# Performance work log

Measured on AMD Instinct MI355X. Metric: run time of the kernel, lower is better.

Reference implementation:

```python
import jax, jax.numpy as jnp
import numpy as np

N_NODES = 50000
N_EDGES = 800000
D = 128
L = 3


def setup_inputs() -> dict:
    key = jax.random.key(0)
    ks = jax.random.split(key, 16)
    x = jax.random.normal(ks[0], (N_NODES, D), dtype=jnp.float32)
    edge_index = jax.random.randint(ks[1], (2, N_EDGES), 0, N_NODES, dtype=jnp.int32)
    # ensure every node has at least one incoming edge (degree > 0)
    edge_index = edge_index.at[1, :N_NODES].set(jnp.arange(N_NODES, dtype=jnp.int32))
    edge_attr = jax.random.normal(ks[2], (N_EDGES, 1), dtype=jnp.float32)
    s = 1.0 / np.sqrt(D)
    lin_w = jax.random.normal(ks[3], (L, 1, D), dtype=jnp.float32)          # edge_dim=1 -> D
    lin_b = jax.random.normal(ks[4], (L, D), dtype=jnp.float32) * s
    eps = jnp.zeros((L,), dtype=jnp.float32)                                 # initial_eps = 0, trainable
    w1 = jax.random.normal(ks[5], (L, D, D), dtype=jnp.float32) * s
    b1 = jax.random.normal(ks[6], (L, D), dtype=jnp.float32) * s
    w2 = jax.random.normal(ks[7], (L, D, D), dtype=jnp.float32) * s
    b2 = jax.random.normal(ks[8], (L, D), dtype=jnp.float32) * s
    d_cat = D + L * D
    final_w = jax.random.normal(ks[9], (d_cat, D), dtype=jnp.float32) / np.sqrt(d_cat)
    final_b = jax.random.normal(ks[10], (D,), dtype=jnp.float32) * s
    return {"x": x, "edge_index": edge_index, "edge_attr": edge_attr,
            "lin_w": lin_w, "lin_b": lin_b, "eps": eps,
            "w1": w1, "b1": b1, "w2": w2, "b2": b2,
            "final_w": final_w, "final_b": final_b}


def reference(x, edge_index, edge_attr, lin_w, lin_b, eps, w1, b1, w2, b2, final_w, final_b):
    src, tgt = edge_index[0], edge_index[1]
    n = x.shape[0]
    # degree of target nodes (float), shape [N, 1]
    deg = jax.ops.segment_sum(jnp.ones(src.shape[0], x.dtype), tgt, num_segments=n)[:, None]
    xs = [x]
    h = x
    for l in range(L):
        e = edge_attr @ lin_w[l] + lin_b[l]                  # [E, D] edge-feature projection
        msg = jax.nn.relu(h[src] + e)                        # gather + fuse + relu
        agg = jax.ops.segment_sum(msg, tgt, num_segments=n)  # scatter-add
        out = agg / deg + (1.0 + eps[l]) * h                 # degree-normalize + eps-residual
        h = jax.nn.relu(out @ w1[l] + b1[l]) @ w2[l] + b2[l] # 2-layer MLP (no BN, no dropout)
        xs.append(h)
    cat = jnp.concatenate(xs, axis=-1)                       # [N, D + L*D]
    return cat @ final_w + final_b
```

## Files before the change

### kernel.cpp

```cpp
#include <hip/hip_runtime.h>

#define NN 50000
#define NE 800000
#define DIM 128
#define NLAYERS 3

typedef __attribute__((ext_vector_type(8))) short bf16x8;
typedef __attribute__((ext_vector_type(4))) float f32x4;

__device__ __forceinline__ unsigned short f2bf_hi(float f) {
    unsigned int u = __float_as_uint(f);
    u += 0x7FFF + ((u >> 16) & 1);
    return (unsigned short)(u >> 16);
}
__device__ __forceinline__ float bf2f(unsigned short u) {
    return __uint_as_float(((unsigned int)u) << 16);
}

__global__ __launch_bounds__(256) void rank_kernel(const int* __restrict__ tgt,
                                                   int* __restrict__ counts,
                                                   int* __restrict__ rank, int E) {
    int base = (blockIdx.x * 256 + threadIdx.x) * 4;
    if (base >= E) return;
    int4 t = *(const int4*)(tgt + base);
    int4 r;
    r.x = atomicAdd(&counts[t.x], 1);
    r.y = atomicAdd(&counts[t.y], 1);
    r.z = atomicAdd(&counts[t.z], 1);
    r.w = atomicAdd(&counts[t.w], 1);
    *(int4*)(rank + base) = r;
}

__global__ __launch_bounds__(256) void scan_partial_kernel(const int* __restrict__ counts,
                                                           int* __restrict__ psum, int n) {
    __shared__ int ws[4];
    int b = blockIdx.x, t = threadIdx.x;
    int idx = b * 1024 + t * 4;
    int v = 0;
    if (idx < n) {
        int4 c = *(const int4*)(counts + idx);
        v = c.x + c.y + c.z + c.w;
    }
#pragma unroll
    for (int o = 32; o > 0; o >>= 1) v += __shfl_xor(v, o);
    int lane = t & 63, wid = t >> 6;
    if (lane == 0) ws[wid] = v;
    __syncthreads();
    if (t == 0) psum[b] = ws[0] + ws[1] + ws[2] + ws[3];
}

__global__ __launch_bounds__(64) void scan_small_kernel(const int* __restrict__ psum,
                                                        int* __restrict__ pbase,
                                                        int* __restrict__ offsets,
                                                        int nb, int n) {
    int lane = threadIdx.x;
    int v = (lane < nb) ? psum[lane] : 0;
    int incl = v;
#pragma unroll
    for (int o = 1; o < 64; o <<= 1) {
        int t = __shfl_up(incl, o);
        if (lane >= o) incl += t;
    }
    if (lane < nb) pbase[lane] = incl - v;
    if (lane == 63) offsets[n] = incl;
}

__global__ __launch_bounds__(256) void scan_apply_kernel(const int* __restrict__ counts,
                                                         const int* __restrict__ pbase,
                                                         int* __restrict__ offsets, int n) {
    __shared__ int ws[4];
    int b = blockIdx.x, t = threadIdx.x;
    int lane = t & 63, wid = t >> 6;
    int idx = b * 1024 + t * 4;
    int4 c = make_int4(0, 0, 0, 0);
    if (idx < n) c = *(const int4*)(counts + idx);
    int tsum = c.x + c.y + c.z + c.w;
    int incl = tsum;
#pragma unroll
    for (int o = 1; o < 64; o <<= 1) {
        int tt = __shfl_up(incl, o);
        if (lane >= o) incl += tt;
    }
    if (lane == 63) ws[wid] = incl;
    __syncthreads();
    int wbase = pbase[b];
    for (int w = 0; w < wid; w++) wbase += ws[w];
    if (idx < n) {
        int e0 = wbase + incl - tsum;
        int4 o;
        o.x = e0;
        o.y = e0 + c.x;
        o.z = o.y + c.y;
        o.w = o.z + c.z;
        *(int4*)(offsets + idx) = o;
    }
}

__global__ __launch_bounds__(256) void scatter2_kernel(
    const int* __restrict__ src, const int* __restrict__ tgt,
    const float* __restrict__ ea, const int* __restrict__ rank,
    const int* __restrict__ offsets, int2* __restrict__ sedge, int E) {
    int base = (blockIdx.x * 256 + threadIdx.x) * 4;
    if (base >= E) return;
    int4 s = *(const int4*)(src + base);
    int4 t = *(const int4*)(tgt + base);
    int4 r = *(const int4*)(rank + base);
    float4 a = *(const float4*)(ea + base);
    sedge[offsets[t.x] + r.x] = make_int2(s.x << 8, __float_as_int(a.x));
    sedge[offsets[t.y] + r.y] = make_int2(s.y << 8, __float_as_int(a.y));
    sedge[offsets[t.z] + r.z] = make_int2(s.z << 8, __float_as_int(a.z));
    sedge[offsets[t.w] + r.w] = make_int2(s.w << 8, __float_as_int(a.w));
}

__global__ __launch_bounds__(256) void xcvt_kernel(const float* __restrict__ x,
                                                   unsigned short* __restrict__ xb, int n) {
    int i = (blockIdx.x * 256 + threadIdx.x) * 4;
    if (i >= n) return;
    float4 v = *(const float4*)(x + i);
    ushort4 o;
    o.x = f2bf_hi(v.x); o.y = f2bf_hi(v.y);
    o.z = f2bf_hi(v.z); o.w = f2bf_hi(v.w);
    *(ushort4*)(xb + i) = o;
}

__global__ __launch_bounds__(256, 8) void agg_kernel(
    const unsigned short* __restrict__ hprev, const int* __restrict__ offs,
    const int2* __restrict__ sedge,
    const float* __restrict__ lw, const float* __restrict__ lb,
    const float* __restrict__ epsp, int layer,
    unsigned short* __restrict__ aggh, unsigned short* __restrict__ aggl, int N) {
    int g = threadIdx.x >> 4;
    int r = threadIdx.x & 15;
    int node = blockIdx.x * 16 + g;
    if (node >= N) return;
    int d0 = r * 8;
    float lwv[8], lbv[8];
    *(float4*)&lwv[0] = *(const float4*)(lw + d0);
    *(float4*)&lwv[4] = *(const float4*)(lw + d0 + 4);
    *(float4*)&lbv[0] = *(const float4*)(lb + d0);
    *(float4*)&lbv[4] = *(const float4*)(lb + d0 + 4);
    const char* hb = (const char*)hprev + r * 16;

    int s0 = offs[node], s1 = offs[node + 1];
    int sm = s1 - 1;
    int cnt = s1 - s0;
    float a[8];
#pragma unroll
    for (int c = 0; c < 8; c++) a[c] = 0.f;

    int2 e0 = sedge[s0];
    int2 e1 = sedge[min(s0 + 1, sm)];
    int2 e2 = sedge[min(s0 + 2, sm)];
    int2 e3 = sedge[min(s0 + 3, sm)];
    uint4 h0 = *(const uint4*)(hb + (unsigned)e0.x);
    uint4 h1 = *(const uint4*)(hb + (unsigned)e1.x);
    uint4 h2 = *(const uint4*)(hb + (unsigned)e2.x);

    for (int it = s0; it < s1; ++it) {
        uint4 h3 = *(const uint4*)(hb + (unsigned)e3.x);
        int2 e4 = sedge[min(it + 4, sm)];
        float wgt = __int_as_float(e0.y);
        unsigned uu[4] = {h0.x, h0.y, h0.z, h0.w};
#pragma unroll
        for (int c = 0; c < 4; c++) {
            float f0 = __uint_as_float(uu[c] << 16);
            float f1 = __uint_as_float(uu[c] & 0xffff0000u);
            a[2 * c]     += fmaxf(f0 + fmaf(wgt, lwv[2 * c], lbv[2 * c]), 0.f);
            a[2 * c + 1] += fmaxf(f1 + fmaf(wgt, lwv[2 * c + 1], lbv[2 * c + 1]), 0.f);
        }
        e0 = e1; e1 = e2; e2 = e3; e3 = e4;
        h0 = h1; h1 = h2; h2 = h3;
    }

    float inv = 1.f / (float)cnt;
    float ge = 1.f + epsp[layer];
    uint4 hs = *(const uint4*)(hb + ((unsigned)node << 8));
    unsigned su[4] = {hs.x, hs.y, hs.z, hs.w};
    unsigned short hh[8], hl[8];
#pragma unroll
    for (int c = 0; c < 4; c++) {
        float f0 = __uint_as_float(su[c] << 16);
        float f1 = __uint_as_float(su[c] & 0xffff0000u);
        float v0 = a[2 * c] * inv + ge * f0;
        float v1 = a[2 * c + 1] * inv + ge * f1;
        unsigned short h0v = f2bf_hi(v0), h1v = f2bf_hi(v1);
        hh[2 * c] = h0v; hh[2 * c + 1] = h1v;
        hl[2 * c] = f2bf_hi(v0 - bf2f(h0v));
        hl[2 * c + 1] = f2bf_hi(v1 - bf2f(h1v));
    }
    unsigned short* ph = aggh + (size_t)node * DIM + d0;
    unsigned short* pl = aggl + (size_t)node * DIM + d0;
    *(ushort4*)ph       = *(const ushort4*)&hh[0];
    *(ushort4*)(ph + 4) = *(const ushort4*)&hh[4];
    *(ushort4*)pl       = *(const ushort4*)&hl[0];
    *(ushort4*)(pl + 4) = *(const ushort4*)&hl[4];
}

__device__ __forceinline__ int packidx(int k, int c) {
    return (((k >> 5) << 3) + (c >> 4)) * 512 + (((k >> 3) & 3) << 7) + ((c & 15) << 3) + (k & 7);
}

__global__ __launch_bounds__(256) void wprep_kernel(
    const float* __restrict__ w1, const float* __restrict__ w2, const float* __restrict__ fw,
    unsigned short* __restrict__ w1t_h, unsigned short* __restrict__ w1t_l,
    unsigned short* __restrict__ w2t_h, unsigned short* __restrict__ w2t_l,
    unsigned short* __restrict__ fwt_h, unsigned short* __restrict__ fwt_l) {
    int gid = blockIdx.x * 256 + threadIdx.x;
    float v; int oidx;
    unsigned short *oh, *ol;
    if (gid < 49152) {
        int l = gid >> 14, rem = gid & 16383, k = rem >> 7, c = rem & 127;
        v = w1[gid]; oidx = l * 16384 + packidx(k, c); oh = w1t_h; ol = w1t_l;
    } else if (gid < 98304) {
        int g = gid - 49152;
        int l = g >> 14, rem = g & 16383, k = rem >> 7, c = rem & 127;
        v = w2[g]; oidx = l * 16384 + packidx(k, c); oh = w2t_h; ol = w2t_l;
    } else if (gid < 163840) {
        int g = gid - 98304;
        int k = g >> 7, c = g & 127;
        v = fw[g]; oidx = packidx(k, c); oh = fwt_h; ol = fwt_l;
    } else return;
    unsigned short h = f2bf_hi(v);
    float lo = v - bf2f(h);
    oh[oidx] = h;
    ol[oidx] = f2bf_hi(lo);
}

#define HSTR 136

__global__ __launch_bounds__(256, 4) void mlp_fused(
    const unsigned short* __restrict__ ah_g, const unsigned short* __restrict__ al_g,
    const unsigned short* __restrict__ w1h, const unsigned short* __restrict__ w1l,
    const float* __restrict__ b1,
    const unsigned short* __restrict__ w2h, const unsigned short* __restrict__ w2l,
    const float* __restrict__ b2,
    unsigned short* __restrict__ out, int N) {
    __shared__ unsigned short s_hh[64 * HSTR], s_hl[64 * HSTR];
    int tid = threadIdx.x;
    int lane = tid & 63, w = tid >> 6;
    int q = lane >> 4, lr = lane & 15;
    int wr = w >> 1, wc = w & 1;
    int n0 = blockIdx.x * 64;
    int nb0 = n0 + wc * 32 + lr;

    f32x4 acc[4][2];
#pragma unroll
    for (int i = 0; i < 4; i++)
#pragma unroll
        for (int j = 0; j < 2; j++) acc[i][j] = (f32x4)(0.f);

#pragma unroll
    for (int k0 = 0; k0 < 128; k0 += 32) {
        bf16x8 Bh[2], Bl[2];
#pragma unroll
        for (int j = 0; j < 2; j++) {
            size_t ro = (size_t)min(nb0 + j * 16, N - 1) * DIM + k0 + q * 8;
            Bh[j] = *(const bf16x8*)(ah_g + ro);
            Bl[j] = *(const bf16x8*)(al_g + ro);
        }
#pragma unroll
        for (int i = 0; i < 4; i++) {
            size_t co = ((size_t)((k0 >> 5) * 8 + wr * 4 + i) << 9) + lane * 8;
            bf16x8 Ah = *(const bf16x8*)(w1h + co);
            bf16x8 Al = *(const bf16x8*)(w1l + co);
#pragma unroll
            for (int j = 0; j < 2; j++) {
                acc[i][j] = __builtin_amdgcn_mfma_f32_16x16x32_bf16(Ah, Bh[j], acc[i][j], 0, 0, 0);
                acc[i][j] = __builtin_amdgcn_mfma_f32_16x16x32_bf16(Ah, Bl[j], acc[i][j], 0, 0, 0);
                acc[i][j] = __builtin_amdgcn_mfma_f32_16x16x32_bf16(Al, Bh[j], acc[i][j], 0, 0, 0);
            }
        }
    }

#pragma unroll
    for (int i = 0; i < 4; i++) {
        int hc0 = wr * 64 + i * 16 + q * 4;
        float4 bv = *(const float4*)(b1 + hc0);
        float bvr[4] = {bv.x, bv.y, bv.z, bv.w};
#pragma unroll
        for (int j = 0; j < 2; j++) {
            int nl = wc * 32 + j * 16 + lr;
            unsigned short hh[4], hl[4];
#pragma unroll
            for (int r = 0; r < 4; r++) {
                float v = fmaxf(acc[i][j][r] + bvr[r], 0.f);
                unsigned short h = f2bf_hi(v);
                hh[r] = h;
                hl[r] = f2bf_hi(v - bf2f(h));
            }
            *(ushort4*)&s_hh[nl * HSTR + hc0] = *(const ushort4*)&hh[0];
            *(ushort4*)&s_hl[nl * HSTR + hc0] = *(const ushort4*)&hl[0];
        }
    }
    __syncthreads();

#pragma unroll
    for (int i = 0; i < 4; i++)
#pragma unroll
        for (int j = 0; j < 2; j++) acc[i][j] = (f32x4)(0.f);

#pragma unroll
    for (int k0 = 0; k0 < 128; k0 += 32) {
        bf16x8 Bh[2], Bl[2];
#pragma unroll
        for (int j = 0; j < 2; j++) {
            int so = (wc * 32 + j * 16 + lr) * HSTR + k0 + q * 8;
            Bh[j] = *(const bf16x8*)&s_hh[so];
            Bl[j] = *(const bf16x8*)&s_hl[so];
        }
#pragma unroll
        for (int i = 0; i < 4; i++) {
            size_t co = ((size_t)((k0 >> 5) * 8 + wr * 4 + i) << 9) + lane * 8;
            bf16x8 Ah = *(const bf16x8*)(w2h + co);
            bf16x8 Al = *(const bf16x8*)(w2l + co);
#pragma unroll
            for (int j = 0; j < 2; j++) {
                acc[i][j] = __builtin_amdgcn_mfma_f32_16x16x32_bf16(Ah, Bh[j], acc[i][j], 0, 0, 0);
                acc[i][j] = __builtin_amdgcn_mfma_f32_16x16x32_bf16(Ah, Bl[j], acc[i][j], 0, 0, 0);
                acc[i][j] = __builtin_amdgcn_mfma_f32_16x16x32_bf16(Al, Bh[j], acc[i][j], 0, 0, 0);
            }
        }
    }

#pragma unroll
    for (int i = 0; i < 4; i++) {
        int hc0 = wr * 64 + i * 16 + q * 4;
        float4 bv = *(const float4*)(b2 + hc0);
        float bvr[4] = {bv.x, bv.y, bv.z, bv.w};
#pragma unroll
        for (int j = 0; j < 2; j++) {
            int node = nb0 + j * 16;
            if (node < N) {
                unsigned short o[4];
#pragma unroll
                for (int r = 0; r < 4; r++) o[r] = f2bf_hi(acc[i][j][r] + bvr[r]);
                *(ushort4*)&out[(size_t)node * DIM + hc0] = *(const ushort4*)&o[0];
            }
        }
    }
}

__global__ __launch_bounds__(256, 4) void final_mfma(
    const unsigned short* __restrict__ a0, const unsigned short* __restrict__ a1,
    const unsigned short* __restrict__ a2, const unsigned short* __restrict__ a3,
    const unsigned short* __restrict__ wh, const unsigned short* __restrict__ wl,
    const float* __restrict__ bias, float* __restrict__ out, int N) {
    int tid = threadIdx.x;
    int lane = tid & 63, w = tid >> 6;
    int q = lane >> 4, lr = lane & 15;
    int wr = w >> 1, wc = w & 1;
    int n0 = blockIdx.x * 64;
    int nb0 = n0 + wc * 32 + lr;

    f32x4 acc[4][2];
#pragma unroll
    for (int i = 0; i < 4; i++)
#pragma unroll
        for (int j = 0; j < 2; j++) acc[i][j] = (f32x4)(0.f);

#pragma unroll
    for (int s = 0; s < 4; s++) {
        const unsigned short* asrc = (s == 0) ? a0 : (s == 1) ? a1 : (s == 2) ? a2 : a3;
#pragma unroll
        for (int kk = 0; kk < 128; kk += 32) {
            int k0 = s * 128 + kk;
            bf16x8 B[2];
#pragma unroll
            for (int j = 0; j < 2; j++) {
                size_t ro = (size_t)min(nb0 + j * 16, N - 1) * DIM + kk + q * 8;
                B[j] = *(const bf16x8*)(asrc + ro);
            }
#pragma unroll
            for (int i = 0; i < 4; i++) {
                size_t co = ((size_t)((k0 >> 5) * 8 + wr * 4 + i) << 9) + lane * 8;
                bf16x8 Ah = *(const bf16x8*)(wh + co);
                bf16x8 Al = *(const bf16x8*)(wl + co);
#pragma unroll
                for (int j = 0; j < 2; j++) {
                    acc[i][j] = __builtin_amdgcn_mfma_f32_16x16x32_bf16(Ah, B[j], acc[i][j], 0, 0, 0);
                    acc[i][j] = __builtin_amdgcn_mfma_f32_16x16x32_bf16(Al, B[j], acc[i][j], 0, 0, 0);
                }
            }
        }
    }

#pragma unroll
    for (int i = 0; i < 4; i++) {
        int hc0 = wr * 64 + i * 16 + q * 4;
        float4 bv = *(const float4*)(bias + hc0);
        float bvr[4] = {bv.x, bv.y, bv.z, bv.w};
#pragma unroll
        for (int j = 0; j < 2; j++) {
            int node = nb0 + j * 16;
            if (node < N) {
                float4 o;
                o.x = acc[i][j][0] + bvr[0];
                o.y = acc[i][j][1] + bvr[1];
                o.z = acc[i][j][2] + bvr[2];
                o.w = acc[i][j][3] + bvr[3];
                *(float4*)&out[(size_t)node * DIM + hc0] = o;
            }
        }
    }
}

extern "C" void kernel_launch(void* const* d_in, const int* in_sizes, int n_in,
                              void* d_out, int out_size, void* d_ws, size_t ws_size,
                              hipStream_t stream) {
    const float* x   = (const float*)d_in[0];
    const int* edge_index = (const int*)d_in[1];
    const float* ea  = (const float*)d_in[2];
    const float* lw  = (const float*)d_in[3];
    const float* lb  = (const float*)d_in[4];
    const float* eps = (const float*)d_in[5];
    const float* w1  = (const float*)d_in[6];
    const float* b1  = (const float*)d_in[7];
    const float* w2  = (const float*)d_in[8];
    const float* b2  = (const float*)d_in[9];
    const float* fw  = (const float*)d_in[10];
    const float* fb  = (const float*)d_in[11];
    float* out = (float*)d_out;

    const int N = NN, E = NE;
    const int* src = edge_index;
    const int* tgt = edge_index + E;
    const int NB = (N + 1023) / 1024;

    char* ws = (char*)d_ws;
    size_t off = 0;
    auto alloc = [&](size_t bytes) {
        void* p = ws + off;
        off += (bytes + 255) & ~(size_t)255;
        return p;
    };
    int*   counts  = (int*)alloc((size_t)N * 4);
    int*   offsets = (int*)alloc((size_t)(N + 1) * 4);
    int*   rank    = (int*)alloc((size_t)E * 4);
    int*   psum    = (int*)alloc((size_t)NB * 4);
    int*   pbase   = (int*)alloc((size_t)NB * 4);
    int2*  sedge   = (int2*)alloc((size_t)E * 8);
    unsigned short* w1t_h = (unsigned short*)alloc(49152 * 2);
    unsigned short* w1t_l = (unsigned short*)alloc(49152 * 2);
    unsigned short* w2t_h = (unsigned short*)alloc(49152 * 2);
    unsigned short* w2t_l = (unsigned short*)alloc(49152 * 2);
    unsigned short* fwt_h = (unsigned short*)alloc(65536 * 2);
    unsigned short* fwt_l = (unsigned short*)alloc(65536 * 2);
    unsigned short* xb    = (unsigned short*)alloc((size_t)N * DIM * 2);
    unsigned short* hbuf[3];
    for (int i = 0; i < 3; i++) hbuf[i] = (unsigned short*)alloc((size_t)N * DIM * 2);
    unsigned short* aggh = (unsigned short*)alloc((size_t)N * DIM * 2);
    unsigned short* aggl = (unsigned short*)alloc((size_t)N * DIM * 2);
    (void)ws_size; (void)in_sizes; (void)n_in; (void)out_size;

    hipMemsetAsync(counts, 0, (size_t)N * 4, stream);
    rank_kernel<<<(E / 4 + 255) / 256, 256, 0, stream>>>(tgt, counts, rank, E);
    wprep_kernel<<<640, 256, 0, stream>>>(w1, w2, fw, w1t_h, w1t_l, w2t_h, w2t_l, fwt_h, fwt_l);
    xcvt_kernel<<<(N * DIM / 4 + 255) / 256, 256, 0, stream>>>(x, xb, N * DIM);
    scan_partial_kernel<<<NB, 256, 0, stream>>>(counts, psum, N);
    scan_small_kernel<<<1, 64, 0, stream>>>(psum, pbase, offsets, NB, N);
    scan_apply_kernel<<<NB, 256, 0, stream>>>(counts, pbase, offsets, N);
    scatter2_kernel<<<(E / 4 + 255) / 256, 256, 0, stream>>>(src, tgt, ea, rank, offsets, sedge, E);

    const int GB = (N + 63) / 64;
    const int AB = (N + 15) / 16;
    for (int l = 0; l < NLAYERS; l++) {
        const unsigned short* hin = (l == 0) ? xb : hbuf[l - 1];
        agg_kernel<<<AB, 256, 0, stream>>>(hin, offsets, sedge,
            lw + l * DIM, lb + l * DIM, eps, l, aggh, aggl, N);
        mlp_fused<<<GB, 256, 0, stream>>>(
            aggh, aggl,
            w1t_h + l * 16384, w1t_l + l * 16384, b1 + l * DIM,
            w2t_h + l * 16384, w2t_l + l * 16384, b2 + l * DIM,
            hbuf[l], N);
    }
    final_mfma<<<GB, 256, 0, stream>>>(
        xb, hbuf[0], hbuf[1], hbuf[2], fwt_h, fwt_l, fb, out, N);
}
```

Baseline: 366.8 us.

## Split MLP and final GEMM work across more waves, software-pipeline final loads

mlp_fused now runs 512 threads (8 waves) per 64-node block, so each wave covers 32 output columns instead of 64, halving its accumulator and weight-register footprint, and weight fragments are loaded before the MFMA loop. final_mfma shrinks to 32-node blocks, with each of 4 waves owning 32 output columns. Its K loop is double-buffered so the next tile's loads are issued while the current tile's MFMAs run. The aim is higher occupancy and better latency hiding in the GEMM stages. The cost is more blocks, and every node tile must re-read all weight fragments from cache.

```diff
diff --git a/kernel.cpp b/kernel.cpp
--- a/kernel.cpp
+++ b/kernel.cpp
@@ -228,7 +228,7 @@
 
 #define HSTR 136
 
-__global__ __launch_bounds__(256, 4) void mlp_fused(
+__global__ __launch_bounds__(512, 5) void mlp_fused(
     const unsigned short* __restrict__ ah_g, const unsigned short* __restrict__ al_g,
     const unsigned short* __restrict__ w1h, const unsigned short* __restrict__ w1l,
     const float* __restrict__ b1,
@@ -239,42 +239,48 @@
     int tid = threadIdx.x;
     int lane = tid & 63, w = tid >> 6;
     int q = lane >> 4, lr = lane & 15;
-    int wr = w >> 1, wc = w & 1;
+    int wr = w & 3, wc = w >> 2;
     int n0 = blockIdx.x * 64;
     int nb0 = n0 + wc * 32 + lr;
-
-    f32x4 acc[4][2];
-#pragma unroll
-    for (int i = 0; i < 4; i++)
+    int rowc[2];
+    rowc[0] = min(nb0, N - 1);
+    rowc[1] = min(nb0 + 16, N - 1);
+
+    f32x4 acc[2][2];
+#pragma unroll
+    for (int i = 0; i < 2; i++)
 #pragma unroll
         for (int j = 0; j < 2; j++) acc[i][j] = (f32x4)(0.f);
 
 #pragma unroll
-    for (int k0 = 0; k0 < 128; k0 += 32) {
-        bf16x8 Bh[2], Bl[2];
+    for (int t = 0; t < 4; t++) {
+        int k0 = t * 32;
+        bf16x8 Bh[2], Bl[2], Ah[2], Al[2];
 #pragma unroll
         for (int j = 0; j < 2; j++) {
-            size_t ro = (size_t)min(nb0 + j * 16, N - 1) * DIM + k0 + q * 8;
+            size_t ro = (size_t)rowc[j] * DIM + k0 + q * 8;
             Bh[j] = *(const bf16x8*)(ah_g + ro);
             Bl[j] = *(const bf16x8*)(al_g + ro);
         }
 #pragma unroll
-        for (int i = 0; i < 4; i++) {
-            size_t co = ((size_t)((k0 >> 5) * 8 + wr * 4 + i) << 9) + lane * 8;
-            bf16x8 Ah = *(const bf16x8*)(w1h + co);
-            bf16x8 Al = *(const bf16x8*)(w1l + co);
+        for (int i = 0; i < 2; i++) {
+            size_t co = ((size_t)(t * 8 + wr * 2 + i) << 9) + lane * 8;
+            Ah[i] = *(const bf16x8*)(w1h + co);
+            Al[i] = *(const bf16x8*)(w1l + co);
+        }
+#pragma unroll
+        for (int i = 0; i < 2; i++)
 #pragma unroll
             for (int j = 0; j < 2; j++) {
-                acc[i][j] = __builtin_amdgcn_mfma_f32_16x16x32_bf16(Ah, Bh[j], acc[i][j], 0, 0, 0);
-                acc[i][j] = __builtin_amdgcn_mfma_f32_16x16x32_bf16(Ah, Bl[j], acc[i][j], 0, 0, 0);
-                acc[i][j] = __builtin_amdgcn_mfma_f32_16x16x32_bf16(Al, Bh[j], acc[i][j], 0, 0, 0);
+                acc[i][j] = __builtin_amdgcn_mfma_f32_16x16x32_bf16(Ah[i], Bh[j], acc[i][j], 0, 0, 0);
+                acc[i][j] = __builtin_amdgcn_mfma_f32_16x16x32_bf16(Ah[i], Bl[j], acc[i][j], 0, 0, 0);
+                acc[i][j] = __builtin_amdgcn_mfma_f32_16x16x32_bf16(Al[i], Bh[j], acc[i][j], 0, 0, 0);
             }
-        }
-    }
-
-#pragma unroll
-    for (int i = 0; i < 4; i++) {
-        int hc0 = wr * 64 + i * 16 + q * 4;
+    }
+
+#pragma unroll
+    for (int i = 0; i < 2; i++) {
+        int hc0 = wr * 32 + i * 16 + q * 4;
         float4 bv = *(const float4*)(b1 + hc0);
         float bvr[4] = {bv.x, bv.y, bv.z, bv.w};
 #pragma unroll
@@ -295,13 +301,14 @@
     __syncthreads();
 
 #pragma unroll
-    for (int i = 0; i < 4; i++)
+    for (int i = 0; i < 2; i++)
 #pragma unroll
         for (int j = 0; j < 2; j++) acc[i][j] = (f32x4)(0.f);
 
 #pragma unroll
-    for (int k0 = 0; k0 < 128; k0 += 32) {
-        bf16x8 Bh[2], Bl[2];
+    for (int t = 0; t < 4; t++) {
+        int k0 = t * 32;
+        bf16x8 Bh[2], Bl[2], Ah[2], Al[2];
 #pragma unroll
         for (int j = 0; j < 2; j++) {
             int so = (wc * 32 + j * 16 + lr) * HSTR + k0 + q * 8;
@@ -309,22 +316,24 @@
             Bl[j] = *(const bf16x8*)&s_hl[so];
         }
 #pragma unroll
-        for (int i = 0; i < 4; i++) {
-            size_t co = ((size_t)((k0 >> 5) * 8 + wr * 4 + i) << 9) + lane * 8;
-            bf16x8 Ah = *(const bf16x8*)(w2h + co);
-            bf16x8 Al = *(const bf16x8*)(w2l + co);
+        for (int i = 0; i < 2; i++) {
+            size_t co = ((size_t)(t * 8 + wr * 2 + i) << 9) + lane * 8;
+            Ah[i] = *(const bf16x8*)(w2h + co);
+            Al[i] = *(const bf16x8*)(w2l + co);
+        }
+#pragma unroll
+        for (int i = 0; i < 2; i++)
 #pragma unroll
             for (int j = 0; j < 2; j++) {
-                acc[i][j] = __builtin_amdgcn_mfma_f32_16x16x32_bf16(Ah, Bh[j], acc[i][j], 0, 0, 0);
-                acc[i][j] = __builtin_amdgcn_mfma_f32_16x16x32_bf16(Ah, Bl[j], acc[i][j], 0, 0, 0);
-                acc[i][j] = __builtin_amdgcn_mfma_f32_16x16x32_bf16(Al, Bh[j], acc[i][j], 0, 0, 0);
+                acc[i][j] = __builtin_amdgcn_mfma_f32_16x16x32_bf16(Ah[i], Bh[j], acc[i][j], 0, 0, 0);
+                acc[i][j] = __builtin_amdgcn_mfma_f32_16x16x32_bf16(Ah[i], Bl[j], acc[i][j], 0, 0, 0);
+                acc[i][j] = __builtin_amdgcn_mfma_f32_16x16x32_bf16(Al[i], Bh[j], acc[i][j], 0, 0, 0);
             }
-        }
-    }
-
-#pragma unroll
-    for (int i = 0; i < 4; i++) {
-        int hc0 = wr * 64 + i * 16 + q * 4;
+    }
+
+#pragma unroll
+    for (int i = 0; i < 2; i++) {
+        int hc0 = wr * 32 + i * 16 + q * 4;
         float4 bv = *(const float4*)(b2 + hc0);
         float bvr[4] = {bv.x, bv.y, bv.z, bv.w};
 #pragma unroll
@@ -340,7 +349,33 @@
     }
 }
 
-__global__ __launch_bounds__(256, 4) void final_mfma(
+#define FIN_LOAD(T, Bv_, Ah_, Al_) do {                                     \
+    const unsigned short* asrc_ = srcs[(T) >> 2];                           \
+    int kk_ = ((T) & 3) * 32;                                               \
+    _Pragma("unroll")                                                       \
+    for (int j_ = 0; j_ < 2; j_++) {                                        \
+        size_t ro_ = (size_t)rowc[j_] * DIM + kk_ + q * 8;                  \
+        Bv_[j_] = *(const bf16x8*)(asrc_ + ro_);                            \
+    }                                                                       \
+    _Pragma("unroll")                                                       \
+    for (int i_ = 0; i_ < 2; i_++) {                                        \
+        size_t co_ = ((size_t)((T) * 8 + w * 2 + i_) << 9) + lane * 8;      \
+        Ah_[i_] = *(const bf16x8*)(wh + co_);                               \
+        Al_[i_] = *(const bf16x8*)(wl + co_);                               \
+    }                                                                       \
+} while (0)
+
+#define FIN_MFMA(Bv_, Ah_, Al_) do {                                        \
+    _Pragma("unroll")                                                       \
+    for (int i_ = 0; i_ < 2; i_++)                                          \
+        _Pragma("unroll")                                                   \
+        for (int j_ = 0; j_ < 2; j_++) {                                    \
+            acc[i_][j_] = __builtin_amdgcn_mfma_f32_16x16x32_bf16(Ah_[i_], Bv_[j_], acc[i_][j_], 0, 0, 0); \
+            acc[i_][j_] = __builtin_amdgcn_mfma_f32_16x16x32_bf16(Al_[i_], Bv_[j_], acc[i_][j_], 0, 0, 0); \
+        }                                                                   \
+} while (0)
+
+__global__ __launch_bounds__(256, 6) void final_mfma(
     const unsigned short* __restrict__ a0, const unsigned short* __restrict__ a1,
     const unsigned short* __restrict__ a2, const unsigned short* __restrict__ a3,
     const unsigned short* __restrict__ wh, const unsigned short* __restrict__ wl,
@@ -348,45 +383,35 @@
     int tid = threadIdx.x;
     int lane = tid & 63, w = tid >> 6;
     int q = lane >> 4, lr = lane & 15;
-    int wr = w >> 1, wc = w & 1;
-    int n0 = blockIdx.x * 64;
-    int nb0 = n0 + wc * 32 + lr;
-
-    f32x4 acc[4][2];
-#pragma unroll
-    for (int i = 0; i < 4; i++)
+    int n0 = blockIdx.x * 32;
+    int nb0 = n0 + lr;
+    const unsigned short* srcs[4] = {a0, a1, a2, a3};
+    int rowc[2];
+    rowc[0] = min(nb0, N - 1);
+    rowc[1] = min(nb0 + 16, N - 1);
+
+    f32x4 acc[2][2];
+#pragma unroll
+    for (int i = 0; i < 2; i++)
 #pragma unroll
         for (int j = 0; j < 2; j++) acc[i][j] = (f32x4)(0.f);
 
-#pragma unroll
-    for (int s = 0; s < 4; s++) {
-        const unsigned short* asrc = (s == 0) ? a0 : (s == 1) ? a1 : (s == 2) ? a2 : a3;
-#pragma unroll
-        for (int kk = 0; kk < 128; kk += 32) {
-            int k0 = s * 128 + kk;
-            bf16x8 B[2];
-#pragma unroll
-            for (int j = 0; j < 2; j++) {
-                size_t ro = (size_t)min(nb0 + j * 16, N - 1) * DIM + kk + q * 8;
-                B[j] = *(const bf16x8*)(asrc + ro);
-            }
-#pragma unroll
-            for (int i = 0; i < 4; i++) {
-                size_t co = ((size_t)((k0 >> 5) * 8 + wr * 4 + i) << 9) + lane * 8;
-                bf16x8 Ah = *(const bf16x8*)(wh + co);
-                bf16x8 Al = *(const bf16x8*)(wl + co);
-#pragma unroll
-                for (int j = 0; j < 2; j++) {
-                    acc[i][j] = __builtin_amdgcn_mfma_f32_16x16x32_bf16(Ah, B[j], acc[i][j], 0, 0, 0);
-                    acc[i][j] = __builtin_amdgcn_mfma_f32_16x16x32_bf16(Al, B[j], acc[i][j], 0, 0, 0);
-                }
-            }
-        }
-    }
-
-#pragma unroll
-    for (int i = 0; i < 4; i++) {
-        int hc0 = wr * 64 + i * 16 + q * 4;
+    bf16x8 pB[2], pAh[2], pAl[2];
+    bf16x8 qB[2], qAh[2], qAl[2];
+
+    FIN_LOAD(0, pB, pAh, pAl);
+    FIN_LOAD(1, qB, qAh, qAl);
+#pragma unroll
+    for (int t = 0; t < 16; t += 2) {
+        FIN_MFMA(pB, pAh, pAl);
+        if (t + 2 < 16) FIN_LOAD(t + 2, pB, pAh, pAl);
+        FIN_MFMA(qB, qAh, qAl);
+        if (t + 3 < 16) FIN_LOAD(t + 3, qB, qAh, qAl);
+    }
+
+#pragma unroll
+    for (int i = 0; i < 2; i++) {
+        int hc0 = w * 32 + i * 16 + q * 4;
         float4 bv = *(const float4*)(bias + hc0);
         float bvr[4] = {bv.x, bv.y, bv.z, bv.w};
 #pragma unroll
@@ -463,16 +488,17 @@
 
     const int GB = (N + 63) / 64;
     const int AB = (N + 15) / 16;
+    const int FB = (N + 31) / 32;
     for (int l = 0; l < NLAYERS; l++) {
         const unsigned short* hin = (l == 0) ? xb : hbuf[l - 1];
         agg_kernel<<<AB, 256, 0, stream>>>(hin, offsets, sedge,
             lw + l * DIM, lb + l * DIM, eps, l, aggh, aggl, N);
-        mlp_fused<<<GB, 256, 0, stream>>>(
+        mlp_fused<<<GB, 512, 0, stream>>>(
             aggh, aggl,
             w1t_h + l * 16384, w1t_l + l * 16384, b1 + l * DIM,
             w2t_h + l * 16384, w2t_l + l * 16384, b2 + l * DIM,
             hbuf[l], N);
     }
-    final_mfma<<<GB, 256, 0, stream>>>(
+    final_mfma<<<FB, 256, 0, stream>>>(
         xb, hbuf[0], hbuf[1], hbuf[2], fwt_h, fwt_l, fb, out, N);
 }
```

Measured after the change: 394.6 us. +7.6%, slower.
